# Kernel optimization log

Hardware: AMD Instinct MI355X
Metric: run time of the kernel (lower is better)

Reference implementation:

```python
import jax, jax.numpy as jnp
import numpy as np

C = 64          # num_channels
NB = 8          # num_bessel
NE = 10         # num_elements
N_NODES = 20000
N_EDGES = 320000

def _silu_norm():
    # e3nn normalize2mom constant for silu: 1/sqrt(E[silu(Z)^2]), Z~N(0,1)
    x, w = np.polynomial.hermite.hermgauss(100)
    z = np.sqrt(2.0) * x
    f = z / (1.0 + np.exp(-z))
    m2 = float(np.sum(w * f * f) / np.sqrt(np.pi))
    return np.float32(1.0 / np.sqrt(m2))

C_SILU = _silu_norm()
SQRT3 = np.float32(np.sqrt(3.0))
SQRT2 = np.float32(np.sqrt(2.0))
INV_SQRT_C = np.float32(1.0 / np.sqrt(C))
INV_SQRT_2C = np.float32(1.0 / np.sqrt(2 * C))
INV_SQRT_3C = np.float32(1.0 / np.sqrt(3 * C))
INV_SQRT_NB = np.float32(1.0 / np.sqrt(NB))
INV_SQRT_64 = np.float32(1.0 / np.sqrt(64.0))


def setup_inputs() -> dict:
    key = jax.random.key(0)
    ks = jax.random.split(key, 22)
    n = lambda k, s: jax.random.normal(k, s, dtype=jnp.float32)
    return {
        "node_feats": n(ks[0], (N_NODES, 4 * C)),
        "edge_feats": jax.random.uniform(ks[1], (N_EDGES, NB), dtype=jnp.float32),
        "edge_attrs": n(ks[2], (N_EDGES, 4)),
        "iedges": jax.random.randint(ks[3], (N_EDGES,), 0, N_NODES),
        "jedges": jax.random.randint(ks[4], (N_EDGES,), 0, N_NODES),
        "atomic_numbers": jax.random.randint(ks[5], (N_NODES,), 0, NE),
        "Wup0": n(ks[6], (C, C)), "Wup1": n(ks[7], (C, C)),
        "Wm1": n(ks[8], (NB, 64)), "Wm2": n(ks[9], (64, 64)),
        "Wm3": n(ks[10], (64, 64)), "Wm4": n(ks[11], (64, 5 * C)),
        "Wl0": n(ks[12], (2 * C, C)), "Wl1": n(ks[13], (3 * C, C)),
        "Ws0c1": n(ks[14], (NE, 1, C)), "Ws0c2": n(ks[15], (NE, 2, C)),
        "Ws0c3": n(ks[16], (NE, 2, C)),
        "Ws1c1": n(ks[17], (NE, 1, C)), "Ws1c2": n(ks[18], (NE, 1, C)),
        "Ws1c3": n(ks[19], (NE, 2, C)),
        "Wp0": n(ks[20], (C, C)), "Wp1": n(ks[21], (C, C)),
    }


def reference(node_feats, edge_feats, edge_attrs, iedges, jedges, atomic_numbers,
              Wup0, Wup1, Wm1, Wm2, Wm3, Wm4, Wl0, Wl1,
              Ws0c1, Ws0c2, Ws0c3, Ws1c1, Ws1c2, Ws1c3, Wp0, Wp1):
    Nn = node_feats.shape[0]
    # split irreps: C scalars (0e) then C vectors (1e), channel-major layout
    s = node_feats[:, :C]                       # (N, C)
    v = node_feats[:, C:].reshape(Nn, C, 3)     # (N, C, 3)

    # linear_up: per-l channel mixing, fan-in normalized (e3nn o3.Linear)
    s = (s @ Wup0) * INV_SQRT_C
    v = jnp.einsum('ncm,ck->nkm', v, Wup1) * INV_SQRT_C

    # conv_tp_weights: e3nn FullyConnectedNet [8,64,64,64,5C] with silu
    h = jax.nn.silu(edge_feats @ (Wm1 * INV_SQRT_NB)) * C_SILU
    h = jax.nn.silu(h @ (Wm2 * INV_SQRT_64)) * C_SILU
    h = jax.nn.silu(h @ (Wm3 * INV_SQRT_64)) * C_SILU
    tpw = h @ (Wm4 * INV_SQRT_64)               # (E, 5C)

    # gather sender node features per edge
    xs = s[iedges]                              # (E, C)
    xv = v[iedges]                              # (E, C, 3)
    eas = edge_attrs[:, 0:1]                    # (E, 1) scalar edge attr
    eav = edge_attrs[:, 1:4]                    # (E, 3) vector edge attr

    # 5 uvu CG paths (component-normalized e3nn TensorProduct):
    wa, wb = tpw[:, 0:C], tpw[:, C:2 * C]
    wc, wd, we = tpw[:, 2 * C:3 * C], tpw[:, 3 * C:4 * C], tpw[:, 4 * C:5 * C]
    m0 = wa * xs * eas                                              # 0e x 0e -> 0e
    m1 = wb * jnp.einsum('ecm,em->ec', xv, eav) / SQRT3             # 1e x 1e -> 0e
    m2 = (wc * xs)[:, :, None] * eav[:, None, :]                    # 0e x 1e -> 1e
    m3 = (wd * eas)[:, :, None] * xv                                # 1e x 0e -> 1e
    m4 = we[:, :, None] * jnp.cross(xv, eav[:, None, :]) / SQRT2    # 1e x 1e -> 1e

    # scatter-sum messages to receiver nodes
    msg_s = jax.ops.segment_sum(jnp.concatenate([m0, m1], axis=1), jedges, num_segments=Nn)        # (N, 2C)
    msg_v = jax.ops.segment_sum(jnp.concatenate([m2, m3, m4], axis=1), jedges, num_segments=Nn)    # (N, 3C, 3)

    # linear: middle irreps (2C x 0e + 3C x 1e) -> C x (0e + 1e)
    s2 = (msg_s @ Wl0) * INV_SQRT_2C            # (N, C)
    v2 = jnp.einsum('ncm,ck->nkm', msg_v, Wl1) * INV_SQRT_3C  # (N, C, 3)

    # symmetric (ACE/MACE) contraction, correlation=3, element-dependent weights
    w01 = Ws0c1[atomic_numbers, 0]              # (N, C)
    w02 = Ws0c2[atomic_numbers]                 # (N, 2, C)
    w03 = Ws0c3[atomic_numbers]                 # (N, 2, C)
    w11 = Ws1c1[atomic_numbers, 0]
    w12 = Ws1c2[atomic_numbers, 0]
    w13 = Ws1c3[atomic_numbers]
    vv = jnp.sum(v2 * v2, axis=-1)              # (N, C) = |v|^2 per channel
    out_s = (w01 * s2 + w02[:, 0] * s2 * s2 + w02[:, 1] * vv / SQRT3
             + w03[:, 0] * s2 * s2 * s2 + w03[:, 1] * s2 * vv / SQRT3)
    coef_v = w11 + w12 * s2 + w13[:, 0] * s2 * s2 + w13[:, 1] * vv / SQRT3
    out_v = coef_v[:, :, None] * v2             # (N, C, 3)

    # linearproduct
    so = (out_s @ Wp0) * INV_SQRT_C
    vo = jnp.einsum('ncm,ck->nkm', out_v, Wp1) * INV_SQRT_C
    return jnp.concatenate([so, vo.reshape(Nn, 3 * C)], axis=1)   # (N, 4C)
```

## Files before the change

kernel.cpp:

```cpp
#include <hip/hip_runtime.h>


typedef unsigned short u16;
typedef unsigned int u32;
typedef __attribute__((ext_vector_type(8))) short bf16x8;
typedef __attribute__((ext_vector_type(4))) float f32x4;

#define CW_UP0 0
#define CW_UP1 4096
#define CW_M1  8192
#define CW_M2  8704
#define CW_M3  12800
#define CW_M4  16896
#define CW_L0  37376
#define CW_L1  45568
#define CW_P0  57856
#define CW_P1  61952
#define CW_S01 66048
#define CW_S02 66688
#define CW_S03 67968
#define CW_S11 69248
#define CW_S12 69888
#define CW_S13 70528
#define CW_TOTAL 71808

#define C_SILU     1.6765224f
#define INV_SQRT3  0.57735027f
#define INV_SQRT2  0.70710678f
#define SC_L1      0.35355339f
#define SC_L234    0.125f

#define HS16 72
#define NFRAG 116
#define FW0 60
#define FW1 76
#define FP0 100
#define FP1 108

__device__ __forceinline__ float b2f(u16 u) {
  union { u32 i; float f; } x; x.i = ((u32)u) << 16; return x.f;
}
__device__ __forceinline__ u16 f2b(float f) {
  union { float f; u32 i; } x; x.f = f;
  u32 i = x.i;
  u32 r = (i + 0x7fffu + ((i >> 16) & 1u)) >> 16;
  return (u16)r;
}
__device__ __forceinline__ float ldf(const void* p, size_t i, int f32) {
  return f32 ? ((const float*)p)[i] : b2f(((const u16*)p)[i]);
}
__device__ __forceinline__ float silu_n(float x) {
  return C_SILU * x / (1.0f + __expf(-x));
}

__global__ void k_detect(const void* nf, int* flag) {
  __shared__ int cnt;
  if (threadIdx.x == 0) cnt = 0;
  __syncthreads();
  const u16* p = (const u16*)nf;
  int wild = 0;
  for (int i = threadIdx.x; i < 4096; i += 256) {
    float ax = fabsf(b2f(p[i]));
    if (!(ax <= 1e10f) || (ax != 0.f && ax < 1e-10f)) wild++;
  }
  atomicAdd(&cnt, wild);
  __syncthreads();
  if (threadIdx.x == 0) *flag = (cnt > 100) ? 1 : 0;
}

struct WPtrs { const void* p[16]; };

__global__ __launch_bounds__(256) void k_front(
    WPtrs wp, float* __restrict__ cw, u16* __restrict__ bwH,
    u16* __restrict__ bwL, const int* __restrict__ je, int* __restrict__ deg,
    const void* __restrict__ nf, float* __restrict__ sup,
    float* __restrict__ vup, int nN, int nE, int nb0,
    const int* __restrict__ flagp) {
  __shared__ float row[4][256];
  const int f32 = *flagp;
  int bid = blockIdx.x, tid = threadIdx.x;

  if (bid < 281) {
    const int   sizes[16]  = {4096,4096,512,4096,4096,20480,8192,12288,4096,
                              4096,640,1280,1280,640,640,1280};
    const float scales[16] = {0.125f,0.125f,0.35355339f,0.125f,0.125f,0.125f,
                              0.08838835f,0.07216878f,0.125f,0.125f,
                              1.f,1.f,1.f,1.f,1.f,1.f};
    int gid = bid * 256 + tid;
    if (gid >= CW_TOTAL) return;
    int off = gid, seg = 0;
    while (off >= sizes[seg]) { off -= sizes[seg]; seg++; }
    cw[gid] = ldf(wp.p[seg], off, f32) * scales[seg];
  } else if (bid < 513) {
    int gid = (bid - 281) * 256 + tid;
    int f = gid >> 9, idx = gid & 511;
    int l = idx >> 3, j = idx & 7;
    int q = l >> 4, col16 = l & 15;
    float v = 0.f;
    if (f < 4) {
      int k = q * 8 + j, n = f * 16 + col16;
      if (k < 8) v = ldf(wp.p[2], (size_t)k * 64 + n, f32);
    } else if (f < 20) {
      const void* w = (f < 12) ? wp.p[3] : wp.p[4];
      int t = (f < 12) ? f - 4 : f - 12;
      int n = (t >> 1) * 16 + col16, ks = t & 1;
      int k = ks * 32 + q * 8 + j;
      v = ldf(w, (size_t)k * 64 + n, f32);
    } else if (f < 60) {
      int t = f - 20;
      int n = (t >> 1) * 16 + col16, ks = t & 1;
      int k = ks * 32 + q * 8 + j;
      v = ldf(wp.p[5], (size_t)k * 320 + n, f32);
    } else if (f < 76) {
      int t = f - FW0, ks = t >> 2, n = t & 3;
      int k = ks * 32 + q * 8 + j;
      v = ldf(wp.p[6], (size_t)k * 64 + n * 16 + col16, f32) * 0.08838835f;
    } else if (f < 100) {
      int t = f - FW1, ks = t >> 2, n = t & 3;
      int k = ks * 32 + q * 8 + j;
      v = ldf(wp.p[7], (size_t)k * 64 + n * 16 + col16, f32) * 0.07216878f;
    } else if (f < 108) {
      int t = f - FP0, ks = t >> 2, n = t & 3;
      int k = ks * 32 + q * 8 + j;
      v = ldf(wp.p[8], (size_t)k * 64 + n * 16 + col16, f32) * 0.125f;
    } else {
      int t = f - FP1, ks = t >> 2, n = t & 3;
      int k = ks * 32 + q * 8 + j;
      v = ldf(wp.p[9], (size_t)k * 64 + n * 16 + col16, f32) * 0.125f;
    }
    u16 hi = f2b(v);
    u16 lo = f2b(v - b2f(hi));
    size_t o = (size_t)f * 512 + (size_t)l * 8 + j;
    bwH[o] = hi;
    bwL[o] = lo;
  } else if (bid < nb0) {
    int e = (bid - 513) * 256 + tid;
    if (e < nE) atomicAdd(&deg[je[e]], 1);
  } else {
    int w = tid >> 6, l = tid & 63;
    int n = (bid - nb0) * 4 + w;
    bool valid = n < nN;
    int nn = valid ? n : 0;
#pragma unroll
    for (int t = 0; t < 4; t++)
      row[w][t * 64 + l] = ldf(nf, (size_t)nn * 256 + t * 64 + l, f32);
    __syncthreads();
    float sacc = 0.f, v0 = 0.f, v1 = 0.f, v2 = 0.f;
#pragma unroll 8
    for (int c = 0; c < 64; c++) {
      float w0 = ldf(wp.p[0], (size_t)c * 64 + l, f32);
      float w1 = ldf(wp.p[1], (size_t)c * 64 + l, f32);
      sacc += row[w][c] * w0;
      v0 += row[w][64 + c * 3 + 0] * w1;
      v1 += row[w][64 + c * 3 + 1] * w1;
      v2 += row[w][64 + c * 3 + 2] * w1;
    }
    if (valid) {
      sup[(size_t)n * 64 + l] = sacc * 0.125f;
      vup[((size_t)n * 3 + 0) * 64 + l] = v0 * 0.125f;
      vup[((size_t)n * 3 + 1) * 64 + l] = v1 * 0.125f;
      vup[((size_t)n * 3 + 2) * 64 + l] = v2 * 0.125f;
    }
  }
}

__global__ __launch_bounds__(256) void k_scan(const int* __restrict__ deg,
                                              int* __restrict__ offs,
                                              int* __restrict__ cursor, int nN) {
  __shared__ int part[256];
  int t = threadIdx.x;
  int per = (nN + 255) / 256;
  int lo = t * per, hi = (t + 1) * per; if (hi > nN) hi = nN;
  int s = 0;
  for (int i = lo; i < hi; i++) s += deg[i];
  part[t] = s;
  __syncthreads();
  if (t == 0) {
    int run = 0;
    for (int i = 0; i < 256; i++) { int v = part[i]; part[i] = run; run += v; }
    offs[nN] = run;
  }
  __syncthreads();
  int run = part[t];
  for (int i = lo; i < hi; i++) {
    offs[i] = run; cursor[i] = run; run += deg[i];
  }
}

__global__ __launch_bounds__(256) void k_scatter2(
    const int* __restrict__ je, const int* __restrict__ ie,
    const void* __restrict__ ea, const void* __restrict__ ef,
    int* __restrict__ cursor, int* __restrict__ iSlot,
    float4* __restrict__ eaSlot, float4* __restrict__ efSlot, int nE,
    const int* __restrict__ flagp) {
  const int f32 = *flagp;
  int e = blockIdx.x * 256 + threadIdx.x;
  if (e >= nE) return;
  int pos = atomicAdd(&cursor[je[e]], 1);
  iSlot[pos] = ie[e];
  float4 av;
  float4 f0, f1;
  if (f32) {
    av = ((const float4*)ea)[e];
    f0 = ((const float4*)ef)[(size_t)e * 2];
    f1 = ((const float4*)ef)[(size_t)e * 2 + 1];
  } else {
    uint2 r = ((const uint2*)ea)[e];
    av = make_float4(b2f(r.x & 0xffff), b2f(r.x >> 16),
                     b2f(r.y & 0xffff), b2f(r.y >> 16));
    uint4 u = ((const uint4*)ef)[e];
    f0 = make_float4(b2f(u.x & 0xffff), b2f(u.x >> 16),
                     b2f(u.y & 0xffff), b2f(u.y >> 16));
    f1 = make_float4(b2f(u.z & 0xffff), b2f(u.z >> 16),
                     b2f(u.w & 0xffff), b2f(u.w >> 16));
  }
  eaSlot[pos] = av;
  efSlot[(size_t)pos * 2] = f0;
  efSlot[(size_t)pos * 2 + 1] = f1;
}

__global__ __launch_bounds__(192) void k_mlp4(
    const float4* __restrict__ efSlot, const int* __restrict__ offs,
    const u16* __restrict__ bwH, const u16* __restrict__ bwL,
    u16* __restrict__ tpw, int gn0, int gn1, int capEff) {
  __shared__ u16 H[3][64 * HS16];
  int tid = threadIdx.x;
  int w = tid >> 6, l = tid & 63;
  int m = l & 15, q = l >> 4;
  int base = offs[gn0];
  int cnt = offs[gn1] - base;
  int lim = cnt < capEff ? cnt : capEff;
  int tb = (blockIdx.x * 3 + w) * 64;
  if (tb >= lim) return;
  u16* Hw = H[w];

  bf16x8 zero8 = {0,0,0,0,0,0,0,0};
  bf16x8 A1h[4], A1l[4];
#pragma unroll
  for (int t = 0; t < 4; t++) { A1h[t] = zero8; A1l[t] = zero8; }
  if (q == 0) {
#pragma unroll
    for (int t = 0; t < 4; t++) {
      int s = tb + t * 16 + m; if (s > lim - 1) s = lim - 1;
      float4 q0 = efSlot[((size_t)(base + s)) * 2];
      float4 q1 = efSlot[((size_t)(base + s)) * 2 + 1];
      float v[8] = {q0.x, q0.y, q0.z, q0.w, q1.x, q1.y, q1.z, q1.w};
      bf16x8 hi, lo;
#pragma unroll
      for (int j = 0; j < 8; j++) {
        u16 h = f2b(v[j]);
        hi[j] = (short)h;
        lo[j] = (short)f2b(v[j] - b2f(h));
      }
      A1h[t] = hi; A1l[t] = lo;
    }
  }
#pragma unroll
  for (int n = 0; n < 4; n++) {
    bf16x8 Bh = *(const bf16x8*)(bwH + (size_t)n * 512 + (size_t)l * 8);
    bf16x8 Bl = *(const bf16x8*)(bwL + (size_t)n * 512 + (size_t)l * 8);
#pragma unroll
    for (int t = 0; t < 4; t++) {
      f32x4 c = (f32x4){0.f, 0.f, 0.f, 0.f};
      c = __builtin_amdgcn_mfma_f32_16x16x32_bf16(A1h[t], Bh, c, 0, 0, 0);
      c = __builtin_amdgcn_mfma_f32_16x16x32_bf16(A1l[t], Bh, c, 0, 0, 0);
      c = __builtin_amdgcn_mfma_f32_16x16x32_bf16(A1h[t], Bl, c, 0, 0, 0);
#pragma unroll
      for (int r = 0; r < 4; r++)
        Hw[(t * 16 + q * 4 + r) * HS16 + n * 16 + m] =
            f2b(silu_n(c[r] * SC_L1));
    }
  }

#pragma unroll
  for (int layer = 0; layer < 2; layer++) {
    int fragBase = 4 + layer * 8;
    bf16x8 Ah[2][4];
#pragma unroll
    for (int ks = 0; ks < 2; ks++)
#pragma unroll
      for (int t = 0; t < 4; t++)
        Ah[ks][t] = *(const bf16x8*)(Hw + (t * 16 + m) * HS16 + ks * 32 + q * 8);
#pragma unroll
    for (int n = 0; n < 4; n++) {
      bf16x8 B0h = *(const bf16x8*)(bwH + (size_t)(fragBase + n * 2 + 0) * 512 +
                                    (size_t)l * 8);
      bf16x8 B0l = *(const bf16x8*)(bwL + (size_t)(fragBase + n * 2 + 0) * 512 +
                                    (size_t)l * 8);
      bf16x8 B1h = *(const bf16x8*)(bwH + (size_t)(fragBase + n * 2 + 1) * 512 +
                                    (size_t)l * 8);
      bf16x8 B1l = *(const bf16x8*)(bwL + (size_t)(fragBase + n * 2 + 1) * 512 +
                                    (size_t)l * 8);
#pragma unroll
      for (int t = 0; t < 4; t++) {
        f32x4 c = (f32x4){0.f, 0.f, 0.f, 0.f};
        c = __builtin_amdgcn_mfma_f32_16x16x32_bf16(Ah[0][t], B0h, c, 0, 0, 0);
        c = __builtin_amdgcn_mfma_f32_16x16x32_bf16(Ah[0][t], B0l, c, 0, 0, 0);
        c = __builtin_amdgcn_mfma_f32_16x16x32_bf16(Ah[1][t], B1h, c, 0, 0, 0);
        c = __builtin_amdgcn_mfma_f32_16x16x32_bf16(Ah[1][t], B1l, c, 0, 0, 0);
#pragma unroll
        for (int r = 0; r < 4; r++)
          Hw[(t * 16 + q * 4 + r) * HS16 + n * 16 + m] =
              f2b(silu_n(c[r] * SC_L234));
      }
    }
  }

  {
    bf16x8 Ah[2][4];
#pragma unroll
    for (int ks = 0; ks < 2; ks++)
#pragma unroll
      for (int t = 0; t < 4; t++)
        Ah[ks][t] = *(const bf16x8*)(Hw + (t * 16 + m) * HS16 + ks * 32 + q * 8);
    for (int n = 0; n < 20; n++) {
      bf16x8 B0h = *(const bf16x8*)(bwH + (size_t)(20 + n * 2 + 0) * 512 +
                                    (size_t)l * 8);
      bf16x8 B0l = *(const bf16x8*)(bwL + (size_t)(20 + n * 2 + 0) * 512 +
                                    (size_t)l * 8);
      bf16x8 B1h = *(const bf16x8*)(bwH + (size_t)(20 + n * 2 + 1) * 512 +
                                    (size_t)l * 8);
      bf16x8 B1l = *(const bf16x8*)(bwL + (size_t)(20 + n * 2 + 1) * 512 +
                                    (size_t)l * 8);
#pragma unroll
      for (int t = 0; t < 4; t++) {
        f32x4 c = (f32x4){0.f, 0.f, 0.f, 0.f};
        c = __builtin_amdgcn_mfma_f32_16x16x32_bf16(Ah[0][t], B0h, c, 0, 0, 0);
        c = __builtin_amdgcn_mfma_f32_16x16x32_bf16(Ah[0][t], B0l, c, 0, 0, 0);
        c = __builtin_amdgcn_mfma_f32_16x16x32_bf16(Ah[1][t], B1h, c, 0, 0, 0);
        c = __builtin_amdgcn_mfma_f32_16x16x32_bf16(Ah[1][t], B1l, c, 0, 0, 0);
#pragma unroll
        for (int r = 0; r < 4; r++) {
          int srow = tb + t * 16 + q * 4 + r;
          if (srow < lim)
            tpw[(size_t)srow * 320 + n * 16 + m] = f2b(c[r] * SC_L234);
        }
      }
    }
  }
}

__global__ __launch_bounds__(256) void k_gather6(
    const int* __restrict__ iSlot, const float4* __restrict__ eaSlot,
    const int* __restrict__ offs, const float* __restrict__ sup,
    const float* __restrict__ vup, const u16* __restrict__ tpw,
    float* __restrict__ msgS, float* __restrict__ msgV,
    int gn0, int gn1, int capEff) {
  int w = threadIdx.x >> 6, l = threadIdx.x & 63;
  int n = gn0 + blockIdx.x * 4 + w;
  if (n >= gn1) return;
  int gbase = offs[gn0];
  int start = offs[n];
  int deg = offs[n + 1] - start;
  int avail = capEff - (start - gbase);
  int dmax = deg < avail ? deg : avail;
  if (dmax < 0) dmax = 0;

  float as0 = 0.f, as1 = 0.f;
  float av[9];
#pragma unroll
  for (int m = 0; m < 9; m++) av[m] = 0.f;

  for (int c0 = 0; c0 < dmax; c0 += 64) {
    int rem = dmax - c0;
    int cend = rem < 64 ? rem : 64;
    int iA = 0;
    float4 eaA = make_float4(0.f, 0.f, 0.f, 0.f);
    if (l < cend) {
      iA = iSlot[start + c0 + l];
      eaA = eaSlot[start + c0 + l];
    }
    for (int qq = 0; qq < cend; qq++) {
      int i = __shfl(iA, qq);
      float eas = __shfl(eaA.x, qq);
      float ev0 = __shfl(eaA.y, qq);
      float ev1 = __shfl(eaA.z, qq);
      float ev2 = __shfl(eaA.w, qq);
      const u16* tp = tpw + (size_t)(start - gbase + c0 + qq) * 320;
      float wa  = b2f(tp[l]);
      float wbv = b2f(tp[64 + l]);
      float wc  = b2f(tp[128 + l]);
      float wd  = b2f(tp[192 + l]);
      float we_ = b2f(tp[256 + l]);
      float xs  = sup[(size_t)i * 64 + l];
      float xv0 = vup[((size_t)i * 3 + 0) * 64 + l];
      float xv1 = vup[((size_t)i * 3 + 1) * 64 + l];
      float xv2 = vup[((size_t)i * 3 + 2) * 64 + l];
      float dot = xv0 * ev0 + xv1 * ev1 + xv2 * ev2;
      as0 += wa * xs * eas;
      as1 += wbv * dot * INV_SQRT3;
      float wcxs = wc * xs;
      float wde  = wd * eas;
      float wef  = we_ * INV_SQRT2;
      av[0] += wcxs * ev0; av[1] += wcxs * ev1; av[2] += wcxs * ev2;
      av[3] += wde * xv0;  av[4] += wde * xv1;  av[5] += wde * xv2;
      av[6] += wef * (xv1 * ev2 - xv2 * ev1);
      av[7] += wef * (xv2 * ev0 - xv0 * ev2);
      av[8] += wef * (xv0 * ev1 - xv1 * ev0);
    }
  }

  msgS[(size_t)n * 128 + l] = as0;
  msgS[(size_t)n * 128 + 64 + l] = as1;
#pragma unroll
  for (int c = 0; c < 3; c++) {
    msgV[(size_t)n * 576 + c * 192 + l]       = av[c];
    msgV[(size_t)n * 576 + c * 192 + 64 + l]  = av[3 + c];
    msgV[(size_t)n * 576 + c * 192 + 128 + l] = av[6 + c];
  }
}

#define POST_G2(SRC, FB, STORE_S, COMP)                                        \
  {                                                                            \
    __syncthreads();                                                           \
    _Pragma("unroll")                                                          \
    for (int t = 0; t < 4; t++)                                                \
      _Pragma("unroll")                                                        \
      for (int r = 0; r < 4; r++)                                              \
        T[t * 16 + q * 4 + r][w * 16 + m] = SRC[t][r];                         \
    __syncthreads();                                                           \
    f32x4 d[4];                                                                \
    _Pragma("unroll")                                                          \
    for (int t = 0; t < 4; t++) d[t] = (f32x4){0.f, 0.f, 0.f, 0.f};            \
    _Pragma("unroll")                                                          \
    for (int ks = 0; ks < 2; ks++) {                                           \
      bf16x8 Bh = *(const bf16x8*)(bwH + (size_t)(FB + ks * 4 + w) * 512 +     \
                                   (size_t)l * 8);                             \
      bf16x8 Bl = *(const bf16x8*)(bwL + (size_t)(FB + ks * 4 + w) * 512 +     \
                                   (size_t)l * 8);                             \
      _Pragma("unroll")                                                        \
      for (int t = 0; t < 4; t++) {                                            \
        bf16x8 Ah, Al;                                                         \
        _Pragma("unroll")                                                      \
        for (int j = 0; j < 8; j++) {                                          \
          float vx = T[t * 16 + m][ks * 32 + q * 8 + j];                       \
          u16 h = f2b(vx);                                                     \
          Ah[j] = (short)h;                                                    \
          Al[j] = (short)f2b(vx - b2f(h));                                     \
        }                                                                      \
        d[t] = __builtin_amdgcn_mfma_f32_16x16x32_bf16(Ah, Bh, d[t], 0, 0, 0); \
        d[t] = __builtin_amdgcn_mfma_f32_16x16x32_bf16(Al, Bh, d[t], 0, 0, 0); \
        d[t] = __builtin_amdgcn_mfma_f32_16x16x32_bf16(Ah, Bl, d[t], 0, 0, 0); \
      }                                                                        \
    }                                                                          \
    _Pragma("unroll")                                                          \
    for (int t = 0; t < 4; t++)                                                \
      _Pragma("unroll")                                                        \
      for (int r = 0; r < 4; r++) {                                            \
        int node = n0 + t * 16 + q * 4 + r;                                    \
        if (node < nN) {                                                       \
          int ch = w * 16 + m;                                                 \
          size_t basep = (size_t)node * 256;                                   \
          size_t oidx = STORE_S ? (basep + ch) : (basep + 64 + ch * 3 + COMP); \
          if (f32) ((float*)out)[oidx] = d[t][r];                              \
          else ((u16*)out)[oidx] = f2b(d[t][r]);                               \
        }                                                                      \
      }                                                                        \
  }

__global__ __launch_bounds__(256) void k_post(
    const float* __restrict__ msgS, const float* __restrict__ msgV,
    const int* __restrict__ an, const float* __restrict__ cw,
    const u16* __restrict__ bwH, const u16* __restrict__ bwL,
    void* __restrict__ out, int nN, const int* __restrict__ flagp) {
  __shared__ float T[64][69];
  const int f32 = *flagp;
  int tid = threadIdx.x;
  int w = tid >> 6, l = tid & 63;
  int m = l & 15, q = l >> 4;
  int n0 = blockIdx.x * 64;

  f32x4 s2[4];
#pragma unroll
  for (int t = 0; t < 4; t++) s2[t] = (f32x4){0.f, 0.f, 0.f, 0.f};
#pragma unroll
  for (int ks = 0; ks < 4; ks++) {
    bf16x8 Bh = *(const bf16x8*)(bwH + (size_t)(FW0 + ks * 4 + w) * 512 +
                                 (size_t)l * 8);
    bf16x8 Bl = *(const bf16x8*)(bwL + (size_t)(FW0 + ks * 4 + w) * 512 +
                                 (size_t)l * 8);
#pragma unroll
    for (int t = 0; t < 4; t++) {
      int row = n0 + t * 16 + m; if (row > nN - 1) row = nN - 1;
      const float* ap = msgS + (size_t)row * 128 + ks * 32 + q * 8;
      bf16x8 Ah, Al;
#pragma unroll
      for (int j = 0; j < 8; j++) {
        float vx = ap[j];
        u16 h = f2b(vx);
        Ah[j] = (short)h;
        Al[j] = (short)f2b(vx - b2f(h));
      }
      s2[t] = __builtin_amdgcn_mfma_f32_16x16x32_bf16(Ah, Bh, s2[t], 0, 0, 0);
      s2[t] = __builtin_amdgcn_mfma_f32_16x16x32_bf16(Al, Bh, s2[t], 0, 0, 0);
      s2[t] = __builtin_amdgcn_mfma_f32_16x16x32_bf16(Ah, Bl, s2[t], 0, 0, 0);
    }
  }

  f32x4 v2[3][4];
#pragma unroll
  for (int c = 0; c < 3; c++)
#pragma unroll
    for (int t = 0; t < 4; t++) v2[c][t] = (f32x4){0.f, 0.f, 0.f, 0.f};
#pragma unroll
  for (int ks = 0; ks < 6; ks++) {
    bf16x8 Bh = *(const bf16x8*)(bwH + (size_t)(FW1 + ks * 4 + w) * 512 +
                                 (size_t)l * 8);
    bf16x8 Bl = *(const bf16x8*)(bwL + (size_t)(FW1 + ks * 4 + w) * 512 +
                                 (size_t)l * 8);
#pragma unroll
    for (int c = 0; c < 3; c++)
#pragma unroll
      for (int t = 0; t < 4; t++) {
        int row = n0 + t * 16 + m; if (row > nN - 1) row = nN - 1;
        const float* ap = msgV + (size_t)row * 576 + c * 192 + ks * 32 + q * 8;
        bf16x8 Ah, Al;
#pragma unroll
        for (int j = 0; j < 8; j++) {
          float vx = ap[j];
          u16 h = f2b(vx);
          Ah[j] = (short)h;
          Al[j] = (short)f2b(vx - b2f(h));
        }
        v2[c][t] = __builtin_amdgcn_mfma_f32_16x16x32_bf16(Ah, Bh, v2[c][t], 0, 0, 0);
        v2[c][t] = __builtin_amdgcn_mfma_f32_16x16x32_bf16(Al, Bh, v2[c][t], 0, 0, 0);
        v2[c][t] = __builtin_amdgcn_mfma_f32_16x16x32_bf16(Ah, Bl, v2[c][t], 0, 0, 0);
      }
  }

  f32x4 os[4];
  f32x4 ov[3][4];
#pragma unroll
  for (int t = 0; t < 4; t++) {
#pragma unroll
    for (int r = 0; r < 4; r++) {
      int node = n0 + t * 16 + q * 4 + r;
      int nc = node > nN - 1 ? nN - 1 : node;
      int a = an[nc];
      int ch = w * 16 + m;
      float s2v = s2[t][r];
      float va = v2[0][t][r], vb = v2[1][t][r], vc = v2[2][t][r];
      float vv = va * va + vb * vb + vc * vc;
      float w01  = cw[CW_S01 + a * 64 + ch];
      float w02a = cw[CW_S02 + a * 128 + ch];
      float w02b = cw[CW_S02 + a * 128 + 64 + ch];
      float w03a = cw[CW_S03 + a * 128 + ch];
      float w03b = cw[CW_S03 + a * 128 + 64 + ch];
      float w11  = cw[CW_S11 + a * 64 + ch];
      float w12  = cw[CW_S12 + a * 64 + ch];
      float w13a = cw[CW_S13 + a * 128 + ch];
      float w13b = cw[CW_S13 + a * 128 + 64 + ch];
      float s2sq = s2v * s2v;
      float vvs = vv * INV_SQRT3;
      float outs = w01 * s2v + w02a * s2sq + w02b * vvs + w03a * s2sq * s2v +
                   w03b * s2v * vvs;
      float coef = w11 + w12 * s2v + w13a * s2sq + w13b * vvs;
      os[t][r] = outs;
      ov[0][t][r] = coef * va;
      ov[1][t][r] = coef * vb;
      ov[2][t][r] = coef * vc;
    }
  }

  POST_G2(os, FP0, 1, 0)
  POST_G2(ov[0], FP1, 0, 0)
  POST_G2(ov[1], FP1, 0, 1)
  POST_G2(ov[2], FP1, 0, 2)
}

extern "C" void kernel_launch(void* const* d_in, const int* in_sizes, int n_in,
                              void* d_out, int out_size, void* d_ws,
                              size_t ws_size, hipStream_t stream) {
  const void* nf = d_in[0];
  const void* ef = d_in[1];
  const void* ea = d_in[2];
  const int* ie = (const int*)d_in[3];
  const int* je = (const int*)d_in[4];
  const int* an = (const int*)d_in[5];
  int nN = in_sizes[0] / 256;
  int nE = in_sizes[3];

  size_t intCnt = (size_t)3 * nN + 1 + nE;
  intCnt = (intCnt + 3) & ~(size_t)3;
  int* deg    = (int*)d_ws;
  int* offs   = deg + nN;
  int* cursor = offs + nN + 1;
  int* iSlot  = cursor + nN;
  float* cw   = (float*)d_ws + intCnt;
  float* sup  = cw + CW_TOTAL;
  float* vup  = sup + (size_t)nN * 64;
  int* flag   = (int*)(vup + (size_t)nN * 192);
  float* msgS = (float*)(flag + 1);
  float* msgV = msgS + (size_t)nN * 128;

  size_t eaByte = (size_t)((char*)(msgV + (size_t)nN * 576) - (char*)d_ws);
  eaByte = (eaByte + 15) & ~(size_t)15;
  float4* eaSlot = (float4*)((char*)d_ws + eaByte);
  float4* efSlot = eaSlot + nE;
  size_t bwByte = eaByte + (size_t)nE * 16 + (size_t)nE * 32;
  u16* bwH = (u16*)((char*)d_ws + bwByte);
  u16* bwL = bwH + (size_t)NFRAG * 512;
  size_t tpwByte = bwByte + (size_t)NFRAG * 512 * 2 * 2;
  tpwByte = (tpwByte + 15) & ~(size_t)15;
  u16* tpw = (u16*)((char*)d_ws + tpwByte);
  size_t capE = (ws_size > tpwByte) ? (ws_size - tpwByte) / 640 : 0;

  int G = 64;
  int nodesPer = (nN + 63) / 64;
  for (int g = 1; g <= 64; g++) {
    int npg = (nN + g - 1) / g;
    size_t worst = (size_t)npg * nE / nN + 6000;
    if (worst <= capE) { G = g; nodesPer = npg; break; }
  }
  int capEff = (int)((size_t)nodesPer * nE / nN + 6000);
  if ((size_t)capEff > capE) capEff = (int)capE;

  k_detect<<<1, 256, 0, stream>>>(nf, flag);
  hipMemsetAsync(deg, 0, (size_t)nN * sizeof(int), stream);

  WPtrs wp;
  const int widx[16] = {6, 7, 8, 9, 10, 11, 12, 13, 20, 21,
                        14, 15, 16, 17, 18, 19};
  for (int i = 0; i < 16; i++) wp.p[i] = d_in[widx[i]];

  int histNB = (nE + 255) / 256;
  int nb0 = 513 + histNB;
  int nupNB = (nN + 3) / 4;
  k_front<<<nb0 + nupNB, 256, 0, stream>>>(wp, cw, bwH, bwL, je, deg, nf,
                                           sup, vup, nN, nE, nb0, flag);
  k_scan<<<1, 256, 0, stream>>>(deg, offs, cursor, nN);
  k_scatter2<<<(nE + 255) / 256, 256, 0, stream>>>(je, ie, ea, ef, cursor,
                                                   iSlot, eaSlot, efSlot, nE,
                                                   flag);

  for (int g = 0; g < G; g++) {
    int gn0 = g * nodesPer;
    if (gn0 >= nN) break;
    int gn1 = gn0 + nodesPer; if (gn1 > nN) gn1 = nN;
    int mlpBlocks = (capEff + 191) / 192;
    k_mlp4<<<mlpBlocks, 192, 0, stream>>>(efSlot, offs, bwH, bwL, tpw,
                                          gn0, gn1, capEff);
    int gBlocks = (gn1 - gn0 + 3) / 4;
    k_gather6<<<gBlocks, 256, 0, stream>>>(iSlot, eaSlot, offs, sup, vup,
                                           tpw, msgS, msgV, gn0, gn1, capEff);
  }
  int postNB = (nN + 63) / 64;
  k_post<<<postNB, 256, 0, stream>>>(msgS, msgV, an, cw, bwH, bwL, d_out,
                                     nN, flag);
}
```

Measured before the change: 585.5 us.

## Store messages as pre-split bf16 hi/lo and shrink post kernel tiles

The gather kernel now writes its message accumulators already split into bf16 high and low halves, so the post kernel can load MFMA A-fragments directly as 16-byte vectors instead of converting fp32 values element by element. The post kernel processes 16 nodes per block instead of 64, which cuts register and LDS use and launches four times as many blocks. The transpose staging in LDS also holds bf16 hi/lo pairs rather than floats. Message storage bytes are unchanged (two u16 per value), and the gather kernel gains the split work and twice as many store instructions.

```diff
diff --git a/kernel.cpp b/kernel.cpp
--- a/kernel.cpp
+++ b/kernel.cpp
@@ -36,6 +36,7 @@
 #define FW1 76
 #define FP0 100
 #define FP1 108
+#define TP 88
 
 __device__ __forceinline__ float b2f(u16 u) {
   union { u32 i; float f; } x; x.i = ((u32)u) << 16; return x.f;
@@ -344,7 +345,8 @@
     const int* __restrict__ iSlot, const float4* __restrict__ eaSlot,
     const int* __restrict__ offs, const float* __restrict__ sup,
     const float* __restrict__ vup, const u16* __restrict__ tpw,
-    float* __restrict__ msgS, float* __restrict__ msgV,
+    u16* __restrict__ msgSh, u16* __restrict__ msgSl,
+    u16* __restrict__ msgVh, u16* __restrict__ msgVl,
     int gn0, int gn1, int capEff) {
   int w = threadIdx.x >> 6, l = threadIdx.x & 63;
   int n = gn0 + blockIdx.x * 4 + w;
@@ -400,172 +402,146 @@
     }
   }
 
-  msgS[(size_t)n * 128 + l] = as0;
-  msgS[(size_t)n * 128 + 64 + l] = as1;
+  {
+    u16 h0 = f2b(as0), h1 = f2b(as1);
+    msgSh[(size_t)n * 128 + l] = h0;
+    msgSh[(size_t)n * 128 + 64 + l] = h1;
+    msgSl[(size_t)n * 128 + l] = f2b(as0 - b2f(h0));
+    msgSl[(size_t)n * 128 + 64 + l] = f2b(as1 - b2f(h1));
+  }
 #pragma unroll
   for (int c = 0; c < 3; c++) {
-    msgV[(size_t)n * 576 + c * 192 + l]       = av[c];
-    msgV[(size_t)n * 576 + c * 192 + 64 + l]  = av[3 + c];
-    msgV[(size_t)n * 576 + c * 192 + 128 + l] = av[6 + c];
-  }
-}
-
-#define POST_G2(SRC, FB, STORE_S, COMP)                                        \
+#pragma unroll
+    for (int b = 0; b < 3; b++) {
+      float x = av[b * 3 + c];
+      u16 h = f2b(x);
+      size_t o = (size_t)n * 576 + c * 192 + b * 64 + l;
+      msgVh[o] = h;
+      msgVl[o] = f2b(x - b2f(h));
+    }
+  }
+}
+
+__global__ __launch_bounds__(256) void k_post2(
+    const u16* __restrict__ msgSh, const u16* __restrict__ msgSl,
+    const u16* __restrict__ msgVh, const u16* __restrict__ msgVl,
+    const int* __restrict__ an, const float* __restrict__ cw,
+    const u16* __restrict__ bwH, const u16* __restrict__ bwL,
+    void* __restrict__ out, int nN, const int* __restrict__ flagp) {
+  __shared__ u16 Thi[16][TP];
+  __shared__ u16 Tlo[16][TP];
+  const int f32 = *flagp;
+  int tid = threadIdx.x;
+  int w = tid >> 6, l = tid & 63;
+  int m = l & 15, q = l >> 4;
+  int n0 = blockIdx.x * 16;
+  int rowA = n0 + m; if (rowA > nN - 1) rowA = nN - 1;
+
+  f32x4 s2 = (f32x4){0.f, 0.f, 0.f, 0.f};
+#pragma unroll
+  for (int ks = 0; ks < 4; ks++) {
+    bf16x8 Bh = *(const bf16x8*)(bwH + (size_t)(FW0 + ks * 4 + w) * 512 +
+                                 (size_t)l * 8);
+    bf16x8 Bl = *(const bf16x8*)(bwL + (size_t)(FW0 + ks * 4 + w) * 512 +
+                                 (size_t)l * 8);
+    bf16x8 Ah = *(const bf16x8*)(msgSh + (size_t)rowA * 128 + ks * 32 + q * 8);
+    bf16x8 Al = *(const bf16x8*)(msgSl + (size_t)rowA * 128 + ks * 32 + q * 8);
+    s2 = __builtin_amdgcn_mfma_f32_16x16x32_bf16(Ah, Bh, s2, 0, 0, 0);
+    s2 = __builtin_amdgcn_mfma_f32_16x16x32_bf16(Al, Bh, s2, 0, 0, 0);
+    s2 = __builtin_amdgcn_mfma_f32_16x16x32_bf16(Ah, Bl, s2, 0, 0, 0);
+  }
+
+  f32x4 v2[3];
+#pragma unroll
+  for (int c = 0; c < 3; c++) v2[c] = (f32x4){0.f, 0.f, 0.f, 0.f};
+#pragma unroll
+  for (int ks = 0; ks < 6; ks++) {
+    bf16x8 Bh = *(const bf16x8*)(bwH + (size_t)(FW1 + ks * 4 + w) * 512 +
+                                 (size_t)l * 8);
+    bf16x8 Bl = *(const bf16x8*)(bwL + (size_t)(FW1 + ks * 4 + w) * 512 +
+                                 (size_t)l * 8);
+#pragma unroll
+    for (int c = 0; c < 3; c++) {
+      size_t o = (size_t)rowA * 576 + c * 192 + ks * 32 + q * 8;
+      bf16x8 Ah = *(const bf16x8*)(msgVh + o);
+      bf16x8 Al = *(const bf16x8*)(msgVl + o);
+      v2[c] = __builtin_amdgcn_mfma_f32_16x16x32_bf16(Ah, Bh, v2[c], 0, 0, 0);
+      v2[c] = __builtin_amdgcn_mfma_f32_16x16x32_bf16(Al, Bh, v2[c], 0, 0, 0);
+      v2[c] = __builtin_amdgcn_mfma_f32_16x16x32_bf16(Ah, Bl, v2[c], 0, 0, 0);
+    }
+  }
+
+  float os[4], ov0[4], ov1[4], ov2[4];
+#pragma unroll
+  for (int r = 0; r < 4; r++) {
+    int node = n0 + q * 4 + r;
+    int nc = node > nN - 1 ? nN - 1 : node;
+    int a = an[nc];
+    int ch = w * 16 + m;
+    float s2v = s2[r];
+    float va = v2[0][r], vb = v2[1][r], vc = v2[2][r];
+    float vv = va * va + vb * vb + vc * vc;
+    float w01  = cw[CW_S01 + a * 64 + ch];
+    float w02a = cw[CW_S02 + a * 128 + ch];
+    float w02b = cw[CW_S02 + a * 128 + 64 + ch];
+    float w03a = cw[CW_S03 + a * 128 + ch];
+    float w03b = cw[CW_S03 + a * 128 + 64 + ch];
+    float w11  = cw[CW_S11 + a * 64 + ch];
+    float w12  = cw[CW_S12 + a * 64 + ch];
+    float w13a = cw[CW_S13 + a * 128 + ch];
+    float w13b = cw[CW_S13 + a * 128 + 64 + ch];
+    float s2sq = s2v * s2v;
+    float vvs = vv * INV_SQRT3;
+    os[r] = w01 * s2v + w02a * s2sq + w02b * vvs + w03a * s2sq * s2v +
+            w03b * s2v * vvs;
+    float coef = w11 + w12 * s2v + w13a * s2sq + w13b * vvs;
+    ov0[r] = coef * va;
+    ov1[r] = coef * vb;
+    ov2[r] = coef * vc;
+  }
+
+#define POST2_G2(SRC, FB, STORE_S, COMP)                                       \
   {                                                                            \
     __syncthreads();                                                           \
     _Pragma("unroll")                                                          \
-    for (int t = 0; t < 4; t++)                                                \
-      _Pragma("unroll")                                                        \
-      for (int r = 0; r < 4; r++)                                              \
-        T[t * 16 + q * 4 + r][w * 16 + m] = SRC[t][r];                         \
+    for (int r = 0; r < 4; r++) {                                              \
+      float x = SRC[r];                                                        \
+      u16 h = f2b(x);                                                          \
+      Thi[q * 4 + r][w * 16 + m] = h;                                          \
+      Tlo[q * 4 + r][w * 16 + m] = f2b(x - b2f(h));                            \
+    }                                                                          \
     __syncthreads();                                                           \
-    f32x4 d[4];                                                                \
-    _Pragma("unroll")                                                          \
-    for (int t = 0; t < 4; t++) d[t] = (f32x4){0.f, 0.f, 0.f, 0.f};            \
+    f32x4 d = (f32x4){0.f, 0.f, 0.f, 0.f};                                     \
     _Pragma("unroll")                                                          \
     for (int ks = 0; ks < 2; ks++) {                                           \
       bf16x8 Bh = *(const bf16x8*)(bwH + (size_t)(FB + ks * 4 + w) * 512 +     \
                                    (size_t)l * 8);                             \
       bf16x8 Bl = *(const bf16x8*)(bwL + (size_t)(FB + ks * 4 + w) * 512 +     \
                                    (size_t)l * 8);                             \
-      _Pragma("unroll")                                                        \
-      for (int t = 0; t < 4; t++) {                                            \
-        bf16x8 Ah, Al;                                                         \
-        _Pragma("unroll")                                                      \
-        for (int j = 0; j < 8; j++) {                                          \
-          float vx = T[t * 16 + m][ks * 32 + q * 8 + j];                       \
-          u16 h = f2b(vx);                                                     \
-          Ah[j] = (short)h;                                                    \
-          Al[j] = (short)f2b(vx - b2f(h));                                     \
-        }                                                                      \
-        d[t] = __builtin_amdgcn_mfma_f32_16x16x32_bf16(Ah, Bh, d[t], 0, 0, 0); \
-        d[t] = __builtin_amdgcn_mfma_f32_16x16x32_bf16(Al, Bh, d[t], 0, 0, 0); \
-        d[t] = __builtin_amdgcn_mfma_f32_16x16x32_bf16(Ah, Bl, d[t], 0, 0, 0); \
+      bf16x8 Ah = *(const bf16x8*)(&Thi[m][ks * 32 + q * 8]);                  \
+      bf16x8 Al = *(const bf16x8*)(&Tlo[m][ks * 32 + q * 8]);                  \
+      d = __builtin_amdgcn_mfma_f32_16x16x32_bf16(Ah, Bh, d, 0, 0, 0);         \
+      d = __builtin_amdgcn_mfma_f32_16x16x32_bf16(Al, Bh, d, 0, 0, 0);         \
+      d = __builtin_amdgcn_mfma_f32_16x16x32_bf16(Ah, Bl, d, 0, 0, 0);         \
+    }                                                                          \
+    _Pragma("unroll")                                                          \
+    for (int r = 0; r < 4; r++) {                                              \
+      int node = n0 + q * 4 + r;                                               \
+      if (node < nN) {                                                         \
+        int ch = w * 16 + m;                                                   \
+        size_t basep = (size_t)node * 256;                                     \
+        size_t oidx = STORE_S ? (basep + ch) : (basep + 64 + ch * 3 + COMP);   \
+        if (f32) ((float*)out)[oidx] = d[r];                                   \
+        else ((u16*)out)[oidx] = f2b(d[r]);                                    \
       }                                                                        \
     }                                                                          \
-    _Pragma("unroll")                                                          \
-    for (int t = 0; t < 4; t++)                                                \
-      _Pragma("unroll")                                                        \
-      for (int r = 0; r < 4; r++) {                                            \
-        int node = n0 + t * 16 + q * 4 + r;                                    \
-        if (node < nN) {                                                       \
-          int ch = w * 16 + m;                                                 \
-          size_t basep = (size_t)node * 256;                                   \
-          size_t oidx = STORE_S ? (basep + ch) : (basep + 64 + ch * 3 + COMP); \
-          if (f32) ((float*)out)[oidx] = d[t][r];                              \
-          else ((u16*)out)[oidx] = f2b(d[t][r]);                               \
-        }                                                                      \
-      }                                                                        \
-  }
-
-__global__ __launch_bounds__(256) void k_post(
-    const float* __restrict__ msgS, const float* __restrict__ msgV,
-    const int* __restrict__ an, const float* __restrict__ cw,
-    const u16* __restrict__ bwH, const u16* __restrict__ bwL,
-    void* __restrict__ out, int nN, const int* __restrict__ flagp) {
-  __shared__ float T[64][69];
-  const int f32 = *flagp;
-  int tid = threadIdx.x;
-  int w = tid >> 6, l = tid & 63;
-  int m = l & 15, q = l >> 4;
-  int n0 = blockIdx.x * 64;
-
-  f32x4 s2[4];
-#pragma unroll
-  for (int t = 0; t < 4; t++) s2[t] = (f32x4){0.f, 0.f, 0.f, 0.f};
-#pragma unroll
-  for (int ks = 0; ks < 4; ks++) {
-    bf16x8 Bh = *(const bf16x8*)(bwH + (size_t)(FW0 + ks * 4 + w) * 512 +
-                                 (size_t)l * 8);
-    bf16x8 Bl = *(const bf16x8*)(bwL + (size_t)(FW0 + ks * 4 + w) * 512 +
-                                 (size_t)l * 8);
-#pragma unroll
-    for (int t = 0; t < 4; t++) {
-      int row = n0 + t * 16 + m; if (row > nN - 1) row = nN - 1;
-      const float* ap = msgS + (size_t)row * 128 + ks * 32 + q * 8;
-      bf16x8 Ah, Al;
-#pragma unroll
-      for (int j = 0; j < 8; j++) {
-        float vx = ap[j];
-        u16 h = f2b(vx);
-        Ah[j] = (short)h;
-        Al[j] = (short)f2b(vx - b2f(h));
-      }
-      s2[t] = __builtin_amdgcn_mfma_f32_16x16x32_bf16(Ah, Bh, s2[t], 0, 0, 0);
-      s2[t] = __builtin_amdgcn_mfma_f32_16x16x32_bf16(Al, Bh, s2[t], 0, 0, 0);
-      s2[t] = __builtin_amdgcn_mfma_f32_16x16x32_bf16(Ah, Bl, s2[t], 0, 0, 0);
-    }
-  }
-
-  f32x4 v2[3][4];
-#pragma unroll
-  for (int c = 0; c < 3; c++)
-#pragma unroll
-    for (int t = 0; t < 4; t++) v2[c][t] = (f32x4){0.f, 0.f, 0.f, 0.f};
-#pragma unroll
-  for (int ks = 0; ks < 6; ks++) {
-    bf16x8 Bh = *(const bf16x8*)(bwH + (size_t)(FW1 + ks * 4 + w) * 512 +
-                                 (size_t)l * 8);
-    bf16x8 Bl = *(const bf16x8*)(bwL + (size_t)(FW1 + ks * 4 + w) * 512 +
-                                 (size_t)l * 8);
-#pragma unroll
-    for (int c = 0; c < 3; c++)
-#pragma unroll
-      for (int t = 0; t < 4; t++) {
-        int row = n0 + t * 16 + m; if (row > nN - 1) row = nN - 1;
-        const float* ap = msgV + (size_t)row * 576 + c * 192 + ks * 32 + q * 8;
-        bf16x8 Ah, Al;
-#pragma unroll
-        for (int j = 0; j < 8; j++) {
-          float vx = ap[j];
-          u16 h = f2b(vx);
-          Ah[j] = (short)h;
-          Al[j] = (short)f2b(vx - b2f(h));
-        }
-        v2[c][t] = __builtin_amdgcn_mfma_f32_16x16x32_bf16(Ah, Bh, v2[c][t], 0, 0, 0);
-        v2[c][t] = __builtin_amdgcn_mfma_f32_16x16x32_bf16(Al, Bh, v2[c][t], 0, 0, 0);
-        v2[c][t] = __builtin_amdgcn_mfma_f32_16x16x32_bf16(Ah, Bl, v2[c][t], 0, 0, 0);
-      }
-  }
-
-  f32x4 os[4];
-  f32x4 ov[3][4];
-#pragma unroll
-  for (int t = 0; t < 4; t++) {
-#pragma unroll
-    for (int r = 0; r < 4; r++) {
-      int node = n0 + t * 16 + q * 4 + r;
-      int nc = node > nN - 1 ? nN - 1 : node;
-      int a = an[nc];
-      int ch = w * 16 + m;
-      float s2v = s2[t][r];
-      float va = v2[0][t][r], vb = v2[1][t][r], vc = v2[2][t][r];
-      float vv = va * va + vb * vb + vc * vc;
-      float w01  = cw[CW_S01 + a * 64 + ch];
-      float w02a = cw[CW_S02 + a * 128 + ch];
-      float w02b = cw[CW_S02 + a * 128 + 64 + ch];
-      float w03a = cw[CW_S03 + a * 128 + ch];
-      float w03b = cw[CW_S03 + a * 128 + 64 + ch];
-      float w11  = cw[CW_S11 + a * 64 + ch];
-      float w12  = cw[CW_S12 + a * 64 + ch];
-      float w13a = cw[CW_S13 + a * 128 + ch];
-      float w13b = cw[CW_S13 + a * 128 + 64 + ch];
-      float s2sq = s2v * s2v;
-      float vvs = vv * INV_SQRT3;
-      float outs = w01 * s2v + w02a * s2sq + w02b * vvs + w03a * s2sq * s2v +
-                   w03b * s2v * vvs;
-      float coef = w11 + w12 * s2v + w13a * s2sq + w13b * vvs;
-      os[t][r] = outs;
-      ov[0][t][r] = coef * va;
-      ov[1][t][r] = coef * vb;
-      ov[2][t][r] = coef * vc;
-    }
-  }
-
-  POST_G2(os, FP0, 1, 0)
-  POST_G2(ov[0], FP1, 0, 0)
-  POST_G2(ov[1], FP1, 0, 1)
-  POST_G2(ov[2], FP1, 0, 2)
+  }
+
+  POST2_G2(os, FP0, 1, 0)
+  POST2_G2(ov0, FP1, 0, 0)
+  POST2_G2(ov1, FP1, 0, 1)
+  POST2_G2(ov2, FP1, 0, 2)
+#undef POST2_G2
 }
 
 extern "C" void kernel_launch(void* const* d_in, const int* in_sizes, int n_in,
@@ -590,10 +566,15 @@
   float* sup  = cw + CW_TOTAL;
   float* vup  = sup + (size_t)nN * 64;
   int* flag   = (int*)(vup + (size_t)nN * 192);
-  float* msgS = (float*)(flag + 1);
-  float* msgV = msgS + (size_t)nN * 128;
-
-  size_t eaByte = (size_t)((char*)(msgV + (size_t)nN * 576) - (char*)d_ws);
+
+  size_t msgByte = (size_t)((char*)(flag + 1) - (char*)d_ws);
+  msgByte = (msgByte + 15) & ~(size_t)15;
+  u16* msgSh = (u16*)((char*)d_ws + msgByte);
+  u16* msgSl = msgSh + (size_t)nN * 128;
+  u16* msgVh = msgSl + (size_t)nN * 128;
+  u16* msgVl = msgVh + (size_t)nN * 576;
+
+  size_t eaByte = msgByte + (size_t)nN * 1408 * 2;
   eaByte = (eaByte + 15) & ~(size_t)15;
   float4* eaSlot = (float4*)((char*)d_ws + eaByte);
   float4* efSlot = eaSlot + nE;
@@ -642,9 +623,10 @@
                                           gn0, gn1, capEff);
     int gBlocks = (gn1 - gn0 + 3) / 4;
     k_gather6<<<gBlocks, 256, 0, stream>>>(iSlot, eaSlot, offs, sup, vup,
-                                           tpw, msgS, msgV, gn0, gn1, capEff);
-  }
-  int postNB = (nN + 63) / 64;
-  k_post<<<postNB, 256, 0, stream>>>(msgS, msgV, an, cw, bwH, bwL, d_out,
-                                     nN, flag);
-}
+                                           tpw, msgSh, msgSl, msgVh, msgVl,
+                                           gn0, gn1, capEff);
+  }
+  int postNB = (nN + 15) / 16;
+  k_post2<<<postNB, 256, 0, stream>>>(msgSh, msgSl, msgVh, msgVl, an, cw,
+                                      bwH, bwL, d_out, nN, flag);
+}
```

After: 508.9 us. -13.1%, faster.
